# Optimization experiments

Measured on AMD Instinct MI355X. Metric: run time of the kernel, lower is better.

Reference implementation:

```python
import jax, jax.numpy as jnp
import numpy as np

EPS = 1e-5
MAX_NORM = 1.0 - 1e-4

def _artanh(x):
    x = jnp.clip(x, -1.0 + 1e-5, 1.0 - 1e-5)
    return 0.5 * (jnp.log1p(x) - jnp.log1p(-x))

def _norm(x):
    return jnp.sqrt(jnp.maximum(jnp.sum(x * x, axis=-1, keepdims=True), EPS * EPS))

def _project(x):
    # clip points into the Poincare ball (c=1)
    n = _norm(x)
    return x * jnp.minimum(1.0, MAX_NORM / n)

def _logmap0(x):
    n = _norm(x)
    return _artanh(n) * x / n

def _expmap0(v):
    n = _norm(v)
    return jnp.tanh(n) * v / n

def _mobius_add(x, y):
    x2 = jnp.sum(x * x, -1, keepdims=True)
    y2 = jnp.sum(y * y, -1, keepdims=True)
    xy = jnp.sum(x * y, -1, keepdims=True)
    num = (1.0 + 2.0 * xy + y2) * x + (1.0 - x2) * y
    den = 1.0 + 2.0 * xy + x2 * y2
    return num / jnp.maximum(den, EPS)

def _mobius_matvec_all(W, x):
    # x: [B,T,D] on ball, W: [K,D,D] -> [B,T,K,D] (mx = x @ W[k].T for each expert k)
    mx = jnp.einsum('btd,ked->btke', x, W)
    xn = _norm(x)[:, :, None, :]            # [B,T,1,1]
    mn = _norm(mx)                          # [B,T,K,1]
    return jnp.tanh(mn / xn * _artanh(xn)) * mx / mn

def _depthwise_conv1d(x, w, b):
    # x: [B,T,C], w: [C,1,3] depthwise, padding=1
    y = jax.lax.conv_general_dilated(
        jnp.transpose(x, (0, 2, 1)), w, (1,), 'SAME',
        feature_group_count=x.shape[-1],
        dimension_numbers=('NCW', 'OIW', 'NCW'))
    return jnp.transpose(y, (0, 2, 1)) + b

def setup_inputs() -> dict:
    key = jax.random.key(0)
    ks = jax.random.split(key, 10)
    B, T, V, D, K, E, R = 8, 512, 50257, 64, 17, 32, 40
    return {
        'tokens': jax.random.randint(ks[0], (B, T), 0, V),
        'token_embed': 0.02 * jax.random.normal(ks[1], (V, D), jnp.float32),
        'conv_w': 0.3 * jax.random.normal(ks[2], (D, 1, 3), jnp.float32),
        'conv_b': jnp.zeros((D,), jnp.float32),
        'lin_w': 0.1 * jax.random.normal(ks[3], (D, K), jnp.float32),
        'lin_b': jnp.zeros((K,), jnp.float32),
        'exp_W': (1.0 / 8.0) * jax.random.normal(ks[4], (K, D, D), jnp.float32),
        'exp_bias': 0.01 * jax.random.normal(ks[5], (K, D), jnp.float32),
        'ln_gamma': jnp.ones((K, E), jnp.float32),
        'ln_beta': jnp.zeros((K, E), jnp.float32),
        'rel_T': jax.random.normal(ks[6], (R, E, E), jnp.float32),
        'rel_S': jax.random.normal(ks[7], (R, E, E), jnp.float32),
    }

def reference(tokens, token_embed, conv_w, conv_b, lin_w, lin_b,
              exp_W, exp_bias, ln_gamma, ln_beta, rel_T, rel_S):
    B, T = tokens.shape
    h0 = token_embed[tokens]                                  # [B,T,64]
    # TinyPosRouter: depthwise conv -> linear -> log_softmax
    hc = _depthwise_conv1d(h0, conv_w, conv_b)
    logp = jax.nn.log_softmax(hc @ lin_w + lin_b, axis=-1)    # [B,T,17]
    p = jnp.exp(logp)
    # round-trip through tangent space (as in source)
    x = _expmap0(_logmap0(_project(h0)))                      # [B,T,64]
    # all 17 hyperbolic experts, batched
    mv = _mobius_matvec_all(exp_W, x)                         # [B,T,17,64]
    y = _project(_mobius_add(mv, _project(exp_bias)))         # mobius bias add
    yt = _logmap0(y)                                          # tangent [B,T,17,64]
    a, g = jnp.split(yt, 2, axis=-1)
    y_glu = a * jax.nn.sigmoid(g)                             # [B,T,17,32]
    mu = jnp.mean(y_glu, -1, keepdims=True)
    var = jnp.var(y_glu, -1, keepdims=True)
    y_ln = (y_glu - mu) / jnp.sqrt(var + 1e-5) * ln_gamma + ln_beta
    y_out = _expmap0(y_ln)                                    # [B,T,17,32]
    y_avg = jnp.einsum('btke,btk->bte', y_out, p)             # soft routing
    # per-relation biaffine scores
    Th = jnp.einsum('btd,rde->brte', y_avg, rel_T)            # [B,40,T,32]
    Sd = jnp.einsum('btd,rde->brte', y_avg, rel_S)
    scores = jnp.einsum('brid,brjd->brij', Th, Sd) / Th.shape[-1]  # [B,40,T,T]
    score_rel = jnp.max(scores, axis=1)                       # [B,T,T]
    score_rel = jnp.where(jnp.eye(T, dtype=bool)[None], -1e9, score_rel)
    # greedy arborescence approximation: each dependent picks max-scoring head
    tree = jnp.argmax(score_rel, axis=1)                      # [B,T]
    return tree, score_rel, logp
```

## Files before the change

### kernel.cpp

```cpp
#include <hip/hip_runtime.h>
#include <hip/hip_bf16.h>
#include <math.h>

#define EPS   1e-5f
#define EPS2  (1e-5f * 1e-5f)
#define MAXN  (1.0f - 1e-4f)

typedef __attribute__((ext_vector_type(8))) short bf16x8;
typedef __attribute__((ext_vector_type(4))) float f32x4;

__device__ __forceinline__ float artanh_(float x) {
    x = fminf(fmaxf(x, -1.0f + 1e-5f), 1.0f - 1e-5f);
    return 0.5f * __logf((1.0f + x) / (1.0f - x));
}
__device__ __forceinline__ float tanh_pos(float x) {
    float t = __expf(-2.0f * x);
    return (1.0f - t) / (1.0f + t);
}
__device__ __forceinline__ float redw(float v) {
    #pragma unroll
    for (int m = 32; m >= 1; m >>= 1) v += __shfl_xor(v, m);
    return v;
}
__device__ __forceinline__ float red16(float v) {
    v += __shfl_xor(v, 1); v += __shfl_xor(v, 2);
    v += __shfl_xor(v, 4); v += __shfl_xor(v, 8);
    return v;
}
__device__ __forceinline__ float red8(float v) {
    v += __shfl_xor(v, 1); v += __shfl_xor(v, 2); v += __shfl_xor(v, 4);
    return v;
}
__device__ __forceinline__ float sigmoid_(float z) { return 1.0f / (1.0f + __expf(-z)); }
__device__ __forceinline__ ushort f2bf(float f) {
    union { __hip_bfloat16 b; ushort u; } cv;
    cv.b = __float2bfloat16(f);
    return cv.u;
}

__global__ __launch_bounds__(256) void k1_token(
    const int* __restrict__ tokens, const float* __restrict__ emb,
    const float* __restrict__ conv_w, const float* __restrict__ conv_b,
    const float* __restrict__ lin_w, const float* __restrict__ lin_b,
    ushort* __restrict__ x_out, float* __restrict__ xn_out,
    float* __restrict__ p_out, float* __restrict__ logp_out,
    const float* __restrict__ expW, ushort* __restrict__ expWb)
{
    if (blockIdx.x >= 1024) {
        const int k = blockIdx.x - 1024;
        const float* src = expW + k * 4096 + threadIdx.x * 16;
        ushort* dst = expWb + k * 4096 + threadIdx.x * 16;
        #pragma unroll
        for (int i = 0; i < 4; ++i) {
            float4 v = *reinterpret_cast<const float4*>(src + i * 4);
            ushort4 o;
            o.x = f2bf(v.x); o.y = f2bf(v.y); o.z = f2bf(v.z); o.w = f2bf(v.w);
            *reinterpret_cast<ushort4*>(dst + i * 4) = o;
        }
        return;
    }

    const int tok = blockIdx.x * 4 + (threadIdx.x >> 6);
    const int t   = tok & 511;
    const int c   = threadIdx.x & 63;

    const int id0 = tokens[tok];
    float h0 = emb[id0 * 64 + c];
    float hm = 0.0f, hp = 0.0f;
    if (t > 0)   hm = emb[tokens[tok - 1] * 64 + c];
    if (t < 511) hp = emb[tokens[tok + 1] * 64 + c];

    float hc = conv_w[c * 3 + 0] * hm + conv_w[c * 3 + 1] * h0 +
               conv_w[c * 3 + 2] * hp + conv_b[c];

    float myLg = 0.0f;
    #pragma unroll
    for (int j = 0; j < 17; ++j) {
        float v = redw(hc * lin_w[c * 17 + j]);
        if (c == j) myLg = v + lin_b[j];
    }
    float mx = (c < 17) ? myLg : -1e30f;
    #pragma unroll
    for (int m = 32; m >= 1; m >>= 1) mx = fmaxf(mx, __shfl_xor(mx, m));
    float ev = (c < 17) ? __expf(myLg - mx) : 0.0f;
    float se = redw(ev);
    float lse = __logf(se);
    if (c < 17) {
        float lp = myLg - mx - lse;
        logp_out[tok * 17 + c] = lp;
        p_out[tok * 17 + c]    = __expf(lp);
    }

    float n0 = sqrtf(fmaxf(redw(h0 * h0), EPS2));
    float xp = h0 * fminf(1.0f, MAXN / n0);
    float n1 = sqrtf(fmaxf(redw(xp * xp), EPS2));
    float v1 = artanh_(n1) / n1 * xp;
    float n2 = sqrtf(fmaxf(redw(v1 * v1), EPS2));
    float xv = tanh_pos(n2) / n2 * v1;

    x_out[tok * 64 + c] = f2bf(xv);
    float n3 = sqrtf(fmaxf(redw(xv * xv), EPS2));
    if (c == 0) xn_out[tok] = n3;
}

__global__ __launch_bounds__(256) void k2_expert(
    const ushort* __restrict__ xb, const float* __restrict__ xn_in,
    const float* __restrict__ p_in, const ushort* __restrict__ Wb,
    const float* __restrict__ expB, const float* __restrict__ g_in,
    const float* __restrict__ b_in, __hip_bfloat16* __restrict__ yk_out)
{
    __shared__ float mv_s[16][65];

    const int tid = threadIdx.x;
    const int l = tid & 63, w = tid >> 6;
    const int tg = tid >> 4, eg = tid & 15;
    const int k = blockIdx.x >> 8;
    const int chunk = blockIdx.x & 255;
    const int tok0 = chunk * 16;

    {
        const int d0 = (l >> 4) * 8;
        const ushort* ap = xb + (tok0 + (l & 15)) * 64 + d0;
        const ushort* bp = Wb + k * 4096 + (16 * w + (l & 15)) * 64 + d0;
        bf16x8 a0 = *reinterpret_cast<const bf16x8*>(ap);
        bf16x8 a1 = *reinterpret_cast<const bf16x8*>(ap + 32);
        bf16x8 b0 = *reinterpret_cast<const bf16x8*>(bp);
        bf16x8 b1 = *reinterpret_cast<const bf16x8*>(bp + 32);
        f32x4 acc = {0.f, 0.f, 0.f, 0.f};
        acc = __builtin_amdgcn_mfma_f32_16x16x32_bf16(a0, b0, acc, 0, 0, 0);
        acc = __builtin_amdgcn_mfma_f32_16x16x32_bf16(a1, b1, acc, 0, 0, 0);
        #pragma unroll
        for (int q = 0; q < 4; ++q)
            mv_s[(l >> 4) * 4 + q][16 * w + (l & 15)] = acc[q];
    }

    float wv = expB[k * 64 + l];
    float s  = redw(wv * wv);
    float nB = sqrtf(fmaxf(s, EPS2));
    float scB = fminf(1.0f, MAXN / nB);
    float y2 = s * scB * scB;
    float pb0 = __shfl(wv, eg * 4 + 0) * scB;
    float pb1 = __shfl(wv, eg * 4 + 1) * scB;
    float pb2 = __shfl(wv, eg * 4 + 2) * scB;
    float pb3 = __shfl(wv, eg * 4 + 3) * scB;

    const int c0 = 4 * (eg & 7);
    float4 gq = *reinterpret_cast<const float4*>(g_in + k * 32 + c0);
    float4 bq = *reinterpret_cast<const float4*>(b_in + k * 32 + c0);
    float pk  = p_in[(tok0 + tg) * 17 + k];
    float xnv = xn_in[tok0 + tg];
    float axnv = artanh_(xnv);

    __syncthreads();

    float4 mvq = *reinterpret_cast<const float4*>(&mv_s[tg][eg * 4]);
    float mv0 = mvq.x, mv1 = mvq.y, mv2 = mvq.z, mv3 = mvq.w;

    float mn = sqrtf(fmaxf(red16(mv0*mv0 + mv1*mv1 + mv2*mv2 + mv3*mv3), EPS2));
    float tv = tanh_pos(mn / xnv * axnv);
    float cf = tv / mn;
    float xa0 = cf * mv0, xa1 = cf * mv1, xa2 = cf * mv2, xa3 = cf * mv3;
    float x2 = tv * tv;

    float xy = red16(xa0*pb0 + xa1*pb1 + xa2*pb2 + xa3*pb3);
    float ca = 1.0f + 2.0f * xy + y2;
    float cb = 1.0f - x2;
    float den = fmaxf(1.0f + 2.0f * xy + x2 * y2, EPS);
    float rden = 1.0f / den;
    float y0 = (ca * xa0 + cb * pb0) * rden;
    float y1 = (ca * xa1 + cb * pb1) * rden;
    float y2c = (ca * xa2 + cb * pb2) * rden;
    float y3 = (ca * xa3 + cb * pb3) * rden;

    float s2 = red16(y0*y0 + y1*y1 + y2c*y2c + y3*y3);
    float nP = sqrtf(fmaxf(s2, EPS2));
    float scP = fminf(1.0f, MAXN / nP);
    y0 *= scP; y1 *= scP; y2c *= scP; y3 *= scP;

    float n2 = sqrtf(fmaxf(s2 * scP * scP, EPS2));
    float lc = artanh_(n2) / n2;
    float yt0 = lc * y0, yt1 = lc * y1, yt2 = lc * y2c, yt3 = lc * y3;

    float pr0 = __shfl_xor(yt0, 8), pr1 = __shfl_xor(yt1, 8);
    float pr2 = __shfl_xor(yt2, 8), pr3 = __shfl_xor(yt3, 8);
    float gl0, gl1, gl2, gl3;
    if (eg < 8) {
        gl0 = yt0 * sigmoid_(pr0); gl1 = yt1 * sigmoid_(pr1);
        gl2 = yt2 * sigmoid_(pr2); gl3 = yt3 * sigmoid_(pr3);
    } else {
        gl0 = pr0 * sigmoid_(yt0); gl1 = pr1 * sigmoid_(yt1);
        gl2 = pr2 * sigmoid_(yt2); gl3 = pr3 * sigmoid_(yt3);
    }

    float mu = red8(gl0 + gl1 + gl2 + gl3) * (1.0f / 32.0f);
    float sq = red8(gl0*gl0 + gl1*gl1 + gl2*gl2 + gl3*gl3) * (1.0f / 32.0f);
    float rstd = rsqrtf(fmaxf(sq - mu * mu, 0.0f) + 1e-5f);
    float ln0 = (gl0 - mu) * rstd * gq.x + bq.x;
    float ln1 = (gl1 - mu) * rstd * gq.y + bq.y;
    float ln2 = (gl2 - mu) * rstd * gq.z + bq.z;
    float ln3 = (gl3 - mu) * rstd * gq.w + bq.w;

    float n3 = sqrtf(fmaxf(red8(ln0*ln0 + ln1*ln1 + ln2*ln2 + ln3*ln3), EPS2));
    float tc = tanh_pos(n3) / n3;

    float wq = pk * tc;

    if (eg < 8) {
        int tok = tok0 + tg;
        ushort4 o;
        o.x = f2bf(wq * ln0);
        o.y = f2bf(wq * ln1);
        o.z = f2bf(wq * ln2);
        o.w = f2bf(wq * ln3);
        *reinterpret_cast<ushort4*>(
            reinterpret_cast<ushort*>(yk_out) + ((size_t)tok * 17 + k) * 32 + c0) = o;
    }
}

__global__ __launch_bounds__(256) void k3_reduce(
    const __hip_bfloat16* __restrict__ yk, ushort* __restrict__ yab)
{
    int idx = blockIdx.x * 256 + threadIdx.x;
    int tok = idx >> 5, e = idx & 31;
    const __hip_bfloat16* p = yk + (size_t)tok * 17 * 32 + e;
    float s = 0.0f;
    #pragma unroll
    for (int k = 0; k < 17; ++k) s += __bfloat162float(p[k * 32]);
    yab[idx] = f2bf(s);
}

__global__ __launch_bounds__(256) void k4_rel(
    const ushort* __restrict__ yab, const float* __restrict__ relT,
    const float* __restrict__ relS, ushort* __restrict__ Z,
    unsigned long long* __restrict__ pmax)
{
    const int blk = blockIdx.x;
    const int b = blk / 160;
    const int rem = blk % 160;
    const int r = rem >> 2, tq = rem & 3;
    __shared__ float Ts[32][33], Ss[32][33], Mm[32][33];
    __shared__ float Zb[128][33];
    const int tid = threadIdx.x;
    const int l = tid & 63, w = tid >> 6;

    if (r == 0 && tid < 128)
        pmax[(size_t)b * 512 + tq * 128 + tid] = 0ull;

    {
        int d = tid >> 3, e0 = (tid & 7) * 4;
        float4 wT = *reinterpret_cast<const float4*>(&relT[r * 1024 + tid * 4]);
        float4 wS = *reinterpret_cast<const float4*>(&relS[r * 1024 + tid * 4]);
        Ts[d][e0 + 0] = wT.x; Ts[d][e0 + 1] = wT.y;
        Ts[d][e0 + 2] = wT.z; Ts[d][e0 + 3] = wT.w;
        Ss[d][e0 + 0] = wS.x; Ss[d][e0 + 1] = wS.y;
        Ss[d][e0 + 2] = wS.z; Ss[d][e0 + 3] = wS.w;
    }
    __syncthreads();

    {
        int d = tid >> 3, dp0 = (tid & 7) * 4;
        float m0 = 0.f, m1 = 0.f, m2 = 0.f, m3 = 0.f;
        #pragma unroll
        for (int e = 0; e < 32; ++e) {
            float tvv = Ts[d][e];
            m0 = fmaf(tvv, Ss[dp0 + 0][e], m0);
            m1 = fmaf(tvv, Ss[dp0 + 1][e], m1);
            m2 = fmaf(tvv, Ss[dp0 + 2][e], m2);
            m3 = fmaf(tvv, Ss[dp0 + 3][e], m3);
        }
        Mm[d][dp0 + 0] = m0; Mm[d][dp0 + 1] = m1;
        Mm[d][dp0 + 2] = m2; Mm[d][dp0 + 3] = m3;
    }
    __syncthreads();

    bf16x8 bm0, bm1;
    #pragma unroll
    for (int i = 0; i < 8; ++i) {
        int d = (l >> 4) * 8 + i;
        bm0[i] = (short)f2bf(Mm[d][(l & 15)]);
        bm1[i] = (short)f2bf(Mm[d][16 + (l & 15)]);
    }

    #pragma unroll
    for (int s = 0; s < 2; ++s) {
        int trow = tq * 128 + (w * 2 + s) * 16 + (l & 15);
        bf16x8 a = *reinterpret_cast<const bf16x8*>(
            yab + ((size_t)(b * 512) + trow) * 32 + (l >> 4) * 8);
        f32x4 acc0 = {0.f, 0.f, 0.f, 0.f}, acc1 = {0.f, 0.f, 0.f, 0.f};
        acc0 = __builtin_amdgcn_mfma_f32_16x16x32_bf16(a, bm0, acc0, 0, 0, 0);
        acc1 = __builtin_amdgcn_mfma_f32_16x16x32_bf16(a, bm1, acc1, 0, 0, 0);
        #pragma unroll
        for (int q = 0; q < 4; ++q) {
            int lr = (w * 2 + s) * 16 + (l >> 4) * 4 + q;
            Zb[lr][(l & 15)]      = acc0[q];
            Zb[lr][16 + (l & 15)] = acc1[q];
        }
    }
    __syncthreads();

    {
        int t2 = tid >> 1, half = tid & 1;
        union { ushort u[16]; uint4 q[2]; } pk;
        #pragma unroll
        for (int j = 0; j < 16; ++j) pk.u[j] = f2bf(Zb[t2][half * 16 + j]);
        size_t off = ((size_t)(b * 40 + r) * 512 + tq * 128 + t2) * 32 + half * 16;
        *reinterpret_cast<uint4*>(Z + off)     = pk.q[0];
        *reinterpret_cast<uint4*>(Z + off + 8) = pk.q[1];
    }
}

__global__ __launch_bounds__(1024) void k5_scores(
    const ushort* __restrict__ Z, const ushort* __restrict__ yab,
    float* __restrict__ score_out, unsigned long long* __restrict__ pmax)
{
    __shared__ float L[4][64][64];
    __shared__ unsigned long long pk_s[16][64];

    const int blk = blockIdx.x;
    const int b = blk >> 6, tile = blk & 63;
    const int it = (tile >> 3) * 64, jt = (tile & 7) * 64;
    const int w = threadIdx.x >> 6, lane = threadIdx.x & 63;
    const int q = w >> 2, s = w & 3;
    const int i0 = it + s * 16;
    const int arow = i0 + (lane & 15);
    const int koff = (lane >> 4) * 8;

    bf16x8 bb[4];
    #pragma unroll
    for (int c = 0; c < 4; ++c) {
        int jrow = jt + c * 16 + (lane & 15);
        bb[c] = *reinterpret_cast<const bf16x8*>(
            yab + ((size_t)(b * 512) + jrow) * 32 + koff);
    }

    f32x4 runmax[4];
    #pragma unroll
    for (int c = 0; c < 4; ++c)
        #pragma unroll
        for (int qq = 0; qq < 4; ++qq) runmax[c][qq] = -3.0e38f;

    const int r0 = q * 10;
    #pragma unroll 2
    for (int r = r0; r < r0 + 10; ++r) {
        bf16x8 a = *reinterpret_cast<const bf16x8*>(
            Z + ((size_t)(b * 40 + r) * 512 + arow) * 32 + koff);
        #pragma unroll
        for (int c = 0; c < 4; ++c) {
            f32x4 acc = {0.f, 0.f, 0.f, 0.f};
            acc = __builtin_amdgcn_mfma_f32_16x16x32_bf16(a, bb[c], acc, 0, 0, 0);
            #pragma unroll
            for (int qq = 0; qq < 4; ++qq) runmax[c][qq] = fmaxf(runmax[c][qq], acc[qq]);
        }
    }

    #pragma unroll
    for (int c = 0; c < 4; ++c) {
        #pragma unroll
        for (int qq = 0; qq < 4; ++qq) {
            int li = s * 16 + (lane >> 4) * 4 + qq;
            int lj = c * 16 + (lane & 15);
            L[q][li][lj] = runmax[c][qq];
        }
    }
    __syncthreads();

    {
        const int jl = threadIdx.x & 63, ig = threadIdx.x >> 6;
        const int gj = jt + jl;
        float bestv = -3.0e38f; int besti = it;
        #pragma unroll
        for (int p = 0; p < 4; ++p) {
            int i = ig + p * 16;
            float v = fmaxf(fmaxf(L[0][i][jl], L[1][i][jl]),
                            fmaxf(L[2][i][jl], L[3][i][jl])) * (1.0f / 32.0f);
            int gi = it + i;
            if (gi == gj) v = -1e9f;
            score_out[((size_t)b * 512 + gi) * 512 + gj] = v;
            if (v > bestv) { bestv = v; besti = gi; }
        }
        unsigned int ub = __float_as_uint(bestv);
        unsigned int ok = (ub >> 31) ? ~ub : (ub | 0x80000000u);
        pk_s[ig][jl] = ((unsigned long long)ok << 32) | (unsigned int)(511 - besti);
    }
    __syncthreads();
    if (threadIdx.x < 64) {
        unsigned long long best = pk_s[0][threadIdx.x];
        #pragma unroll
        for (int g = 1; g < 16; ++g) {
            unsigned long long v = pk_s[g][threadIdx.x];
            if (v > best) best = v;
        }
        atomicMax(&pmax[(size_t)b * 512 + jt + threadIdx.x], best);
    }
}

__global__ __launch_bounds__(256) void k6_tree(
    const unsigned long long* __restrict__ pmax, float* __restrict__ tree)
{
    int idx = blockIdx.x * 256 + threadIdx.x;
    tree[idx] = (float)(511 - (int)(pmax[idx] & 0x1ffull));
}

extern "C" void kernel_launch(void* const* d_in, const int* in_sizes, int n_in,
                              void* d_out, int out_size, void* d_ws, size_t ws_size,
                              hipStream_t stream)
{
    const int*   tokens  = (const int*)  d_in[0];
    const float* emb     = (const float*)d_in[1];
    const float* conv_w  = (const float*)d_in[2];
    const float* conv_b  = (const float*)d_in[3];
    const float* lin_w   = (const float*)d_in[4];
    const float* lin_b   = (const float*)d_in[5];
    const float* expW    = (const float*)d_in[6];
    const float* expB    = (const float*)d_in[7];
    const float* ln_g    = (const float*)d_in[8];
    const float* ln_b    = (const float*)d_in[9];
    const float* relT    = (const float*)d_in[10];
    const float* relS    = (const float*)d_in[11];

    float* out = (float*)d_out;
    float* tree_out  = out;
    float* score_out = out + 4096;
    float* logp_out  = out + 4096 + 2097152;

    float* ws = (float*)d_ws;
    ushort* xb_ws  = (ushort*)ws;
    float*  xn_ws  = ws + 131072;
    float*  p_ws   = ws + 135168;
    ushort* Wb_ws  = (ushort*)(ws + 204800);
    ushort* yab_ws = (ushort*)(ws + 239616);
    __hip_bfloat16* yk_ws = (__hip_bfloat16*)(ws + 305152);
    ushort* Z_ws   = (ushort*)(ws + 1419264);
    unsigned long long* pmax_ws =
        (unsigned long long*)(ws + 4040704);

    k1_token<<<1041, 256, 0, stream>>>(tokens, emb, conv_w, conv_b, lin_w, lin_b,
                                       xb_ws, xn_ws, p_ws, logp_out, expW, Wb_ws);
    k2_expert<<<4352, 256, 0, stream>>>(xb_ws, xn_ws, p_ws, Wb_ws, expB, ln_g, ln_b, yk_ws);
    k3_reduce<<<512, 256, 0, stream>>>(yk_ws, yab_ws);
    k4_rel<<<1280, 256, 0, stream>>>(yab_ws, relT, relS, Z_ws, pmax_ws);
    k5_scores<<<512, 1024, 0, stream>>>(Z_ws, yab_ws, score_out, pmax_ws);
    k6_tree<<<16, 256, 0, stream>>>(pmax_ws, tree_out);
}
```

Baseline: 60.63 us.

## Fuse expert reduction into consumers and fold tree extraction into score kernel

Removes the separate expert-sum kernel: the relation and score kernels each recompute the 17-expert sum for their token tile directly from the per-expert outputs. Each relation block now handles two relations, halving the grid and amortizing the recomputed reduction. The final tree extraction moves into the score kernel via a per-batch completion counter, so the last block writes the argmax. This removes two launches and an intermediate buffer, but adds redundant reduction reads and relies on atomic counter ordering.

```diff
diff --git a/kernel.cpp b/kernel.cpp
--- a/kernel.cpp
+++ b/kernel.cpp
@@ -217,120 +217,138 @@
     }
 }
 
-__global__ __launch_bounds__(256) void k3_reduce(
-    const __hip_bfloat16* __restrict__ yk, ushort* __restrict__ yab)
-{
-    int idx = blockIdx.x * 256 + threadIdx.x;
-    int tok = idx >> 5, e = idx & 31;
-    const __hip_bfloat16* p = yk + (size_t)tok * 17 * 32 + e;
-    float s = 0.0f;
-    #pragma unroll
-    for (int k = 0; k < 17; ++k) s += __bfloat162float(p[k * 32]);
-    yab[idx] = f2bf(s);
-}
-
 __global__ __launch_bounds__(256) void k4_rel(
-    const ushort* __restrict__ yab, const float* __restrict__ relT,
+    const __hip_bfloat16* __restrict__ yk, const float* __restrict__ relT,
     const float* __restrict__ relS, ushort* __restrict__ Z,
-    unsigned long long* __restrict__ pmax)
+    unsigned long long* __restrict__ pmax, unsigned int* __restrict__ cnt)
 {
     const int blk = blockIdx.x;
-    const int b = blk / 160;
-    const int rem = blk % 160;
-    const int r = rem >> 2, tq = rem & 3;
+    const int b = blk / 80;
+    const int rem = blk % 80;
+    const int rp = rem >> 2, tq = rem & 3;
     __shared__ float Ts[32][33], Ss[32][33], Mm[32][33];
     __shared__ float Zb[128][33];
+    __shared__ ushort yas[128][40];
     const int tid = threadIdx.x;
     const int l = tid & 63, w = tid >> 6;
 
-    if (r == 0 && tid < 128)
+    if (rp == 0 && tid < 128)
         pmax[(size_t)b * 512 + tq * 128 + tid] = 0ull;
-
-    {
-        int d = tid >> 3, e0 = (tid & 7) * 4;
-        float4 wT = *reinterpret_cast<const float4*>(&relT[r * 1024 + tid * 4]);
-        float4 wS = *reinterpret_cast<const float4*>(&relS[r * 1024 + tid * 4]);
-        Ts[d][e0 + 0] = wT.x; Ts[d][e0 + 1] = wT.y;
-        Ts[d][e0 + 2] = wT.z; Ts[d][e0 + 3] = wT.w;
-        Ss[d][e0 + 0] = wS.x; Ss[d][e0 + 1] = wS.y;
-        Ss[d][e0 + 2] = wS.z; Ss[d][e0 + 3] = wS.w;
-    }
-    __syncthreads();
-
-    {
-        int d = tid >> 3, dp0 = (tid & 7) * 4;
-        float m0 = 0.f, m1 = 0.f, m2 = 0.f, m3 = 0.f;
-        #pragma unroll
-        for (int e = 0; e < 32; ++e) {
-            float tvv = Ts[d][e];
-            m0 = fmaf(tvv, Ss[dp0 + 0][e], m0);
-            m1 = fmaf(tvv, Ss[dp0 + 1][e], m1);
-            m2 = fmaf(tvv, Ss[dp0 + 2][e], m2);
-            m3 = fmaf(tvv, Ss[dp0 + 3][e], m3);
-        }
-        Mm[d][dp0 + 0] = m0; Mm[d][dp0 + 1] = m1;
-        Mm[d][dp0 + 2] = m2; Mm[d][dp0 + 3] = m3;
-    }
-    __syncthreads();
-
-    bf16x8 bm0, bm1;
-    #pragma unroll
-    for (int i = 0; i < 8; ++i) {
-        int d = (l >> 4) * 8 + i;
-        bm0[i] = (short)f2bf(Mm[d][(l & 15)]);
-        bm1[i] = (short)f2bf(Mm[d][16 + (l & 15)]);
-    }
-
-    #pragma unroll
-    for (int s = 0; s < 2; ++s) {
-        int trow = tq * 128 + (w * 2 + s) * 16 + (l & 15);
-        bf16x8 a = *reinterpret_cast<const bf16x8*>(
-            yab + ((size_t)(b * 512) + trow) * 32 + (l >> 4) * 8);
-        f32x4 acc0 = {0.f, 0.f, 0.f, 0.f}, acc1 = {0.f, 0.f, 0.f, 0.f};
-        acc0 = __builtin_amdgcn_mfma_f32_16x16x32_bf16(a, bm0, acc0, 0, 0, 0);
-        acc1 = __builtin_amdgcn_mfma_f32_16x16x32_bf16(a, bm1, acc1, 0, 0, 0);
-        #pragma unroll
-        for (int q = 0; q < 4; ++q) {
-            int lr = (w * 2 + s) * 16 + (l >> 4) * 4 + q;
-            Zb[lr][(l & 15)]      = acc0[q];
-            Zb[lr][16 + (l & 15)] = acc1[q];
-        }
-    }
-    __syncthreads();
-
-    {
-        int t2 = tid >> 1, half = tid & 1;
-        union { ushort u[16]; uint4 q[2]; } pk;
-        #pragma unroll
-        for (int j = 0; j < 16; ++j) pk.u[j] = f2bf(Zb[t2][half * 16 + j]);
-        size_t off = ((size_t)(b * 40 + r) * 512 + tq * 128 + t2) * 32 + half * 16;
-        *reinterpret_cast<uint4*>(Z + off)     = pk.q[0];
-        *reinterpret_cast<uint4*>(Z + off + 8) = pk.q[1];
+    if (rem == 0 && tid == 128)
+        cnt[b] = 0u;
+
+    for (int i = tid; i < 4096; i += 256) {
+        int row = i >> 5, e = i & 31;
+        const __hip_bfloat16* p =
+            yk + ((size_t)(b * 512 + tq * 128 + row) * 17) * 32 + e;
+        float s = 0.0f;
+        #pragma unroll
+        for (int k = 0; k < 17; ++k) s += __bfloat162float(p[k * 32]);
+        yas[row][e] = f2bf(s);
+    }
+
+    for (int rr = 2 * rp; rr <= 2 * rp + 1; ++rr) {
+        __syncthreads();
+
+        {
+            int d = tid >> 3, e0 = (tid & 7) * 4;
+            float4 wT = *reinterpret_cast<const float4*>(&relT[rr * 1024 + tid * 4]);
+            float4 wS = *reinterpret_cast<const float4*>(&relS[rr * 1024 + tid * 4]);
+            Ts[d][e0 + 0] = wT.x; Ts[d][e0 + 1] = wT.y;
+            Ts[d][e0 + 2] = wT.z; Ts[d][e0 + 3] = wT.w;
+            Ss[d][e0 + 0] = wS.x; Ss[d][e0 + 1] = wS.y;
+            Ss[d][e0 + 2] = wS.z; Ss[d][e0 + 3] = wS.w;
+        }
+        __syncthreads();
+
+        {
+            int d = tid >> 3, dp0 = (tid & 7) * 4;
+            float m0 = 0.f, m1 = 0.f, m2 = 0.f, m3 = 0.f;
+            #pragma unroll
+            for (int e = 0; e < 32; ++e) {
+                float tvv = Ts[d][e];
+                m0 = fmaf(tvv, Ss[dp0 + 0][e], m0);
+                m1 = fmaf(tvv, Ss[dp0 + 1][e], m1);
+                m2 = fmaf(tvv, Ss[dp0 + 2][e], m2);
+                m3 = fmaf(tvv, Ss[dp0 + 3][e], m3);
+            }
+            Mm[d][dp0 + 0] = m0; Mm[d][dp0 + 1] = m1;
+            Mm[d][dp0 + 2] = m2; Mm[d][dp0 + 3] = m3;
+        }
+        __syncthreads();
+
+        bf16x8 bm0, bm1;
+        #pragma unroll
+        for (int i = 0; i < 8; ++i) {
+            int d = (l >> 4) * 8 + i;
+            bm0[i] = (short)f2bf(Mm[d][(l & 15)]);
+            bm1[i] = (short)f2bf(Mm[d][16 + (l & 15)]);
+        }
+
+        #pragma unroll
+        for (int s = 0; s < 2; ++s) {
+            int lrow = (w * 2 + s) * 16 + (l & 15);
+            bf16x8 a = *reinterpret_cast<const bf16x8*>(&yas[lrow][(l >> 4) * 8]);
+            f32x4 acc0 = {0.f, 0.f, 0.f, 0.f}, acc1 = {0.f, 0.f, 0.f, 0.f};
+            acc0 = __builtin_amdgcn_mfma_f32_16x16x32_bf16(a, bm0, acc0, 0, 0, 0);
+            acc1 = __builtin_amdgcn_mfma_f32_16x16x32_bf16(a, bm1, acc1, 0, 0, 0);
+            #pragma unroll
+            for (int q = 0; q < 4; ++q) {
+                int lr = (w * 2 + s) * 16 + (l >> 4) * 4 + q;
+                Zb[lr][(l & 15)]      = acc0[q];
+                Zb[lr][16 + (l & 15)] = acc1[q];
+            }
+        }
+        __syncthreads();
+
+        {
+            int t2 = tid >> 1, half = tid & 1;
+            union { ushort u[16]; uint4 q[2]; } pk;
+            #pragma unroll
+            for (int j = 0; j < 16; ++j) pk.u[j] = f2bf(Zb[t2][half * 16 + j]);
+            size_t off = ((size_t)(b * 40 + rr) * 512 + tq * 128 + t2) * 32 + half * 16;
+            *reinterpret_cast<uint4*>(Z + off)     = pk.q[0];
+            *reinterpret_cast<uint4*>(Z + off + 8) = pk.q[1];
+        }
     }
 }
 
 __global__ __launch_bounds__(1024) void k5_scores(
-    const ushort* __restrict__ Z, const ushort* __restrict__ yab,
-    float* __restrict__ score_out, unsigned long long* __restrict__ pmax)
+    const __hip_bfloat16* __restrict__ yk, const ushort* __restrict__ Z,
+    float* __restrict__ score_out, unsigned long long* __restrict__ pmax,
+    unsigned int* __restrict__ cnt, float* __restrict__ tree)
 {
     __shared__ float L[4][64][64];
     __shared__ unsigned long long pk_s[16][64];
+    __shared__ ushort ybb[64][40];
+    __shared__ unsigned int last_s;
 
     const int blk = blockIdx.x;
     const int b = blk >> 6, tile = blk & 63;
     const int it = (tile >> 3) * 64, jt = (tile & 7) * 64;
-    const int w = threadIdx.x >> 6, lane = threadIdx.x & 63;
+    const int tid = threadIdx.x;
+    const int w = tid >> 6, lane = tid & 63;
     const int q = w >> 2, s = w & 3;
     const int i0 = it + s * 16;
     const int arow = i0 + (lane & 15);
     const int koff = (lane >> 4) * 8;
 
+    for (int i = tid; i < 2048; i += 1024) {
+        int row = i >> 5, e = i & 31;
+        const __hip_bfloat16* p =
+            yk + ((size_t)(b * 512 + jt + row) * 17) * 32 + e;
+        float sv = 0.0f;
+        #pragma unroll
+        for (int k = 0; k < 17; ++k) sv += __bfloat162float(p[k * 32]);
+        ybb[row][e] = f2bf(sv);
+    }
+    __syncthreads();
+
     bf16x8 bb[4];
     #pragma unroll
     for (int c = 0; c < 4; ++c) {
-        int jrow = jt + c * 16 + (lane & 15);
-        bb[c] = *reinterpret_cast<const bf16x8*>(
-            yab + ((size_t)(b * 512) + jrow) * 32 + koff);
+        int lrow = c * 16 + (lane & 15);
+        bb[c] = *reinterpret_cast<const bf16x8*>(&ybb[lrow][koff]);
     }
 
     f32x4 runmax[4];
@@ -365,7 +383,7 @@
     __syncthreads();
 
     {
-        const int jl = threadIdx.x & 63, ig = threadIdx.x >> 6;
+        const int jl = tid & 63, ig = tid >> 6;
         const int gj = jt + jl;
         float bestv = -3.0e38f; int besti = it;
         #pragma unroll
@@ -383,22 +401,23 @@
         pk_s[ig][jl] = ((unsigned long long)ok << 32) | (unsigned int)(511 - besti);
     }
     __syncthreads();
-    if (threadIdx.x < 64) {
-        unsigned long long best = pk_s[0][threadIdx.x];
+    if (tid < 64) {
+        unsigned long long best = pk_s[0][tid];
         #pragma unroll
         for (int g = 1; g < 16; ++g) {
-            unsigned long long v = pk_s[g][threadIdx.x];
+            unsigned long long v = pk_s[g][tid];
             if (v > best) best = v;
         }
-        atomicMax(&pmax[(size_t)b * 512 + jt + threadIdx.x], best);
-    }
-}
-
-__global__ __launch_bounds__(256) void k6_tree(
-    const unsigned long long* __restrict__ pmax, float* __restrict__ tree)
-{
-    int idx = blockIdx.x * 256 + threadIdx.x;
-    tree[idx] = (float)(511 - (int)(pmax[idx] & 0x1ffull));
+        atomicMax(&pmax[(size_t)b * 512 + jt + tid], best);
+    }
+
+    __syncthreads();
+    if (tid == 0) last_s = atomicAdd(&cnt[b], 1u);
+    __syncthreads();
+    if (last_s == 63u && tid < 512) {
+        unsigned long long key = atomicMax(&pmax[(size_t)b * 512 + tid], 0ull);
+        tree[b * 512 + tid] = (float)(511 - (int)(key & 0x1ffull));
+    }
 }
 
 extern "C" void kernel_launch(void* const* d_in, const int* in_sizes, int n_in,
@@ -428,17 +447,15 @@
     float*  xn_ws  = ws + 131072;
     float*  p_ws   = ws + 135168;
     ushort* Wb_ws  = (ushort*)(ws + 204800);
-    ushort* yab_ws = (ushort*)(ws + 239616);
-    __hip_bfloat16* yk_ws = (__hip_bfloat16*)(ws + 305152);
-    ushort* Z_ws   = (ushort*)(ws + 1419264);
+    __hip_bfloat16* yk_ws = (__hip_bfloat16*)(ws + 239616);
+    ushort* Z_ws   = (ushort*)(ws + 1353728);
     unsigned long long* pmax_ws =
-        (unsigned long long*)(ws + 4040704);
+        (unsigned long long*)(ws + 3975168);
+    unsigned int* cnt_ws = (unsigned int*)(ws + 3983360);
 
     k1_token<<<1041, 256, 0, stream>>>(tokens, emb, conv_w, conv_b, lin_w, lin_b,
                                        xb_ws, xn_ws, p_ws, logp_out, expW, Wb_ws);
     k2_expert<<<4352, 256, 0, stream>>>(xb_ws, xn_ws, p_ws, Wb_ws, expB, ln_g, ln_b, yk_ws);
-    k3_reduce<<<512, 256, 0, stream>>>(yk_ws, yab_ws);
-    k4_rel<<<1280, 256, 0, stream>>>(yab_ws, relT, relS, Z_ws, pmax_ws);
-    k5_scores<<<512, 1024, 0, stream>>>(Z_ws, yab_ws, score_out, pmax_ws);
-    k6_tree<<<16, 256, 0, stream>>>(pmax_ws, tree_out);
-}
+    k4_rel<<<640, 256, 0, stream>>>(yk_ws, relT, relS, Z_ws, pmax_ws, cnt_ws);
+    k5_scores<<<512, 1024, 0, stream>>>(yk_ws, Z_ws, score_out, pmax_ws, cnt_ws, tree_out);
+}
```

Result: slower. 68.64 us (+13.2%).

## Keep expert matvec results in MFMA registers, one wave per token-chunk

Applied to the files above, without the earlier changes.

The expert kernel now assigns one wavefront per (expert, 16-token chunk). Each wave computes all four 16-column MFMA tiles itself and runs the hyperbolic/GLU/LayerNorm epilogue straight from the accumulator layout, instead of staging through shared memory with a block barrier. The GLU pairing maps directly onto tile halves, so the cross-lane swap for the gate disappears. The trade is fewer launched blocks, a sequential loop over four tokens per lane, and narrower 2-byte scattered stores in place of ushort4 stores.

```diff
diff --git a/kernel.cpp b/kernel.cpp
--- a/kernel.cpp
+++ b/kernel.cpp
@@ -25,10 +25,6 @@
 __device__ __forceinline__ float red16(float v) {
     v += __shfl_xor(v, 1); v += __shfl_xor(v, 2);
     v += __shfl_xor(v, 4); v += __shfl_xor(v, 8);
-    return v;
-}
-__device__ __forceinline__ float red8(float v) {
-    v += __shfl_xor(v, 1); v += __shfl_xor(v, 2); v += __shfl_xor(v, 4);
     return v;
 }
 __device__ __forceinline__ float sigmoid_(float z) { return 1.0f / (1.0f + __expf(-z)); }
@@ -109,111 +105,89 @@
     const float* __restrict__ expB, const float* __restrict__ g_in,
     const float* __restrict__ b_in, __hip_bfloat16* __restrict__ yk_out)
 {
-    __shared__ float mv_s[16][65];
-
-    const int tid = threadIdx.x;
-    const int l = tid & 63, w = tid >> 6;
-    const int tg = tid >> 4, eg = tid & 15;
-    const int k = blockIdx.x >> 8;
-    const int chunk = blockIdx.x & 255;
+    const int gid = blockIdx.x * 4 + (threadIdx.x >> 6);
+    const int l  = threadIdx.x & 63;
+    const int k  = gid >> 8;
+    const int chunk = gid & 255;
     const int tok0 = chunk * 16;
-
-    {
-        const int d0 = (l >> 4) * 8;
-        const ushort* ap = xb + (tok0 + (l & 15)) * 64 + d0;
-        const ushort* bp = Wb + k * 4096 + (16 * w + (l & 15)) * 64 + d0;
-        bf16x8 a0 = *reinterpret_cast<const bf16x8*>(ap);
-        bf16x8 a1 = *reinterpret_cast<const bf16x8*>(ap + 32);
+    const int lg = l >> 4, li = l & 15;
+    const int d0 = lg * 8;
+
+    const ushort* ap = xb + (tok0 + li) * 64 + d0;
+    bf16x8 a0 = *reinterpret_cast<const bf16x8*>(ap);
+    bf16x8 a1 = *reinterpret_cast<const bf16x8*>(ap + 32);
+
+    f32x4 mv[4];
+    #pragma unroll
+    for (int c = 0; c < 4; ++c) {
+        const ushort* bp = Wb + k * 4096 + (c * 16 + li) * 64 + d0;
         bf16x8 b0 = *reinterpret_cast<const bf16x8*>(bp);
         bf16x8 b1 = *reinterpret_cast<const bf16x8*>(bp + 32);
         f32x4 acc = {0.f, 0.f, 0.f, 0.f};
         acc = __builtin_amdgcn_mfma_f32_16x16x32_bf16(a0, b0, acc, 0, 0, 0);
         acc = __builtin_amdgcn_mfma_f32_16x16x32_bf16(a1, b1, acc, 0, 0, 0);
-        #pragma unroll
-        for (int q = 0; q < 4; ++q)
-            mv_s[(l >> 4) * 4 + q][16 * w + (l & 15)] = acc[q];
+        mv[c] = acc;
     }
 
     float wv = expB[k * 64 + l];
-    float s  = redw(wv * wv);
-    float nB = sqrtf(fmaxf(s, EPS2));
+    float sB = redw(wv * wv);
+    float nB = sqrtf(fmaxf(sB, EPS2));
     float scB = fminf(1.0f, MAXN / nB);
-    float y2 = s * scB * scB;
-    float pb0 = __shfl(wv, eg * 4 + 0) * scB;
-    float pb1 = __shfl(wv, eg * 4 + 1) * scB;
-    float pb2 = __shfl(wv, eg * 4 + 2) * scB;
-    float pb3 = __shfl(wv, eg * 4 + 3) * scB;
-
-    const int c0 = 4 * (eg & 7);
-    float4 gq = *reinterpret_cast<const float4*>(g_in + k * 32 + c0);
-    float4 bq = *reinterpret_cast<const float4*>(b_in + k * 32 + c0);
-    float pk  = p_in[(tok0 + tg) * 17 + k];
-    float xnv = xn_in[tok0 + tg];
-    float axnv = artanh_(xnv);
-
-    __syncthreads();
-
-    float4 mvq = *reinterpret_cast<const float4*>(&mv_s[tg][eg * 4]);
-    float mv0 = mvq.x, mv1 = mvq.y, mv2 = mvq.z, mv3 = mvq.w;
-
-    float mn = sqrtf(fmaxf(red16(mv0*mv0 + mv1*mv1 + mv2*mv2 + mv3*mv3), EPS2));
-    float tv = tanh_pos(mn / xnv * axnv);
-    float cf = tv / mn;
-    float xa0 = cf * mv0, xa1 = cf * mv1, xa2 = cf * mv2, xa3 = cf * mv3;
-    float x2 = tv * tv;
-
-    float xy = red16(xa0*pb0 + xa1*pb1 + xa2*pb2 + xa3*pb3);
-    float ca = 1.0f + 2.0f * xy + y2;
-    float cb = 1.0f - x2;
-    float den = fmaxf(1.0f + 2.0f * xy + x2 * y2, EPS);
-    float rden = 1.0f / den;
-    float y0 = (ca * xa0 + cb * pb0) * rden;
-    float y1 = (ca * xa1 + cb * pb1) * rden;
-    float y2c = (ca * xa2 + cb * pb2) * rden;
-    float y3 = (ca * xa3 + cb * pb3) * rden;
-
-    float s2 = red16(y0*y0 + y1*y1 + y2c*y2c + y3*y3);
-    float nP = sqrtf(fmaxf(s2, EPS2));
-    float scP = fminf(1.0f, MAXN / nP);
-    y0 *= scP; y1 *= scP; y2c *= scP; y3 *= scP;
-
-    float n2 = sqrtf(fmaxf(s2 * scP * scP, EPS2));
-    float lc = artanh_(n2) / n2;
-    float yt0 = lc * y0, yt1 = lc * y1, yt2 = lc * y2c, yt3 = lc * y3;
-
-    float pr0 = __shfl_xor(yt0, 8), pr1 = __shfl_xor(yt1, 8);
-    float pr2 = __shfl_xor(yt2, 8), pr3 = __shfl_xor(yt3, 8);
-    float gl0, gl1, gl2, gl3;
-    if (eg < 8) {
-        gl0 = yt0 * sigmoid_(pr0); gl1 = yt1 * sigmoid_(pr1);
-        gl2 = yt2 * sigmoid_(pr2); gl3 = yt3 * sigmoid_(pr3);
-    } else {
-        gl0 = pr0 * sigmoid_(yt0); gl1 = pr1 * sigmoid_(yt1);
-        gl2 = pr2 * sigmoid_(yt2); gl3 = pr3 * sigmoid_(yt3);
-    }
-
-    float mu = red8(gl0 + gl1 + gl2 + gl3) * (1.0f / 32.0f);
-    float sq = red8(gl0*gl0 + gl1*gl1 + gl2*gl2 + gl3*gl3) * (1.0f / 32.0f);
-    float rstd = rsqrtf(fmaxf(sq - mu * mu, 0.0f) + 1e-5f);
-    float ln0 = (gl0 - mu) * rstd * gq.x + bq.x;
-    float ln1 = (gl1 - mu) * rstd * gq.y + bq.y;
-    float ln2 = (gl2 - mu) * rstd * gq.z + bq.z;
-    float ln3 = (gl3 - mu) * rstd * gq.w + bq.w;
-
-    float n3 = sqrtf(fmaxf(red8(ln0*ln0 + ln1*ln1 + ln2*ln2 + ln3*ln3), EPS2));
-    float tc = tanh_pos(n3) / n3;
-
-    float wq = pk * tc;
-
-    if (eg < 8) {
-        int tok = tok0 + tg;
-        ushort4 o;
-        o.x = f2bf(wq * ln0);
-        o.y = f2bf(wq * ln1);
-        o.z = f2bf(wq * ln2);
-        o.w = f2bf(wq * ln3);
-        *reinterpret_cast<ushort4*>(
-            reinterpret_cast<ushort*>(yk_out) + ((size_t)tok * 17 + k) * 32 + c0) = o;
+    float y2 = sB * scB * scB;
+    float pb[4];
+    #pragma unroll
+    for (int c = 0; c < 4; ++c) pb[c] = __shfl(wv, c * 16 + li) * scB;
+
+    float gq0 = g_in[k * 32 + li],      gq1 = g_in[k * 32 + 16 + li];
+    float bq0 = b_in[k * 32 + li],      bq1 = b_in[k * 32 + 16 + li];
+
+    #pragma unroll
+    for (int q = 0; q < 4; ++q) {
+        const int tok = tok0 + lg * 4 + q;
+        float m0 = mv[0][q], m1 = mv[1][q], m2 = mv[2][q], m3 = mv[3][q];
+        float xnv = xn_in[tok];
+        float axnv = artanh_(xnv);
+
+        float mn = sqrtf(fmaxf(red16(m0*m0 + m1*m1 + m2*m2 + m3*m3), EPS2));
+        float tv = tanh_pos(mn / xnv * axnv);
+        float cf = tv / mn;
+        float xa0 = cf * m0, xa1 = cf * m1, xa2 = cf * m2, xa3 = cf * m3;
+        float x2 = tv * tv;
+
+        float xy = red16(xa0*pb[0] + xa1*pb[1] + xa2*pb[2] + xa3*pb[3]);
+        float ca = 1.0f + 2.0f * xy + y2;
+        float cb = 1.0f - x2;
+        float rden = 1.0f / fmaxf(1.0f + 2.0f * xy + x2 * y2, EPS);
+        float y0 = (ca * xa0 + cb * pb[0]) * rden;
+        float y1 = (ca * xa1 + cb * pb[1]) * rden;
+        float y2c = (ca * xa2 + cb * pb[2]) * rden;
+        float y3 = (ca * xa3 + cb * pb[3]) * rden;
+
+        float s2 = red16(y0*y0 + y1*y1 + y2c*y2c + y3*y3);
+        float nP = sqrtf(fmaxf(s2, EPS2));
+        float scP = fminf(1.0f, MAXN / nP);
+        y0 *= scP; y1 *= scP; y2c *= scP; y3 *= scP;
+
+        float n2 = sqrtf(fmaxf(s2 * scP * scP, EPS2));
+        float lc = artanh_(n2) / n2;
+        float yt0 = lc * y0, yt1 = lc * y1, yt2 = lc * y2c, yt3 = lc * y3;
+
+        float gl0 = yt0 * sigmoid_(yt2);
+        float gl1 = yt1 * sigmoid_(yt3);
+
+        float mu = red16(gl0 + gl1) * (1.0f / 32.0f);
+        float sq = red16(gl0*gl0 + gl1*gl1) * (1.0f / 32.0f);
+        float rstd = rsqrtf(fmaxf(sq - mu * mu, 0.0f) + 1e-5f);
+        float ln0 = (gl0 - mu) * rstd * gq0 + bq0;
+        float ln1 = (gl1 - mu) * rstd * gq1 + bq1;
+
+        float n3 = sqrtf(fmaxf(red16(ln0*ln0 + ln1*ln1), EPS2));
+        float tc = tanh_pos(n3) / n3;
+
+        float wq = p_in[tok * 17 + k] * tc;
+        ushort* dst = reinterpret_cast<ushort*>(yk_out) + (size_t)tok * 544 + k * 32;
+        dst[li]      = f2bf(wq * ln0);
+        dst[16 + li] = f2bf(wq * ln1);
     }
 }
 
@@ -436,7 +410,7 @@
 
     k1_token<<<1041, 256, 0, stream>>>(tokens, emb, conv_w, conv_b, lin_w, lin_b,
                                        xb_ws, xn_ws, p_ws, logp_out, expW, Wb_ws);
-    k2_expert<<<4352, 256, 0, stream>>>(xb_ws, xn_ws, p_ws, Wb_ws, expB, ln_g, ln_b, yk_ws);
+    k2_expert<<<1088, 256, 0, stream>>>(xb_ws, xn_ws, p_ws, Wb_ws, expB, ln_g, ln_b, yk_ws);
     k3_reduce<<<512, 256, 0, stream>>>(yk_ws, yab_ws);
     k4_rel<<<1280, 256, 0, stream>>>(yab_ws, relT, relS, Z_ws, pmax_ws);
     k5_scores<<<512, 1024, 0, stream>>>(Z_ws, yab_ws, score_out, pmax_ws);
```

Result: slower. 62.52 us (+3.1%).
